# Optimization experiments

Measured on AMD Instinct MI355X. Metric: run time of the kernel, lower is better.

The kernel has to match this reference:

```python
import math
import jax, jax.numpy as jnp
import numpy as np

B = 16; ENC_S = 64; ENC_T = 96
SCALE = 64; POOL = 16; DM = 256; NH = 16
E_LAYERS = 3; D_LAYERS = 2; DFF = 1024
OUT_S = 64; OUT_T = 32
LN_EPS = 1e-5


def _pe(d_model, length):
    pos = np.arange(length, dtype=np.float32)[:, None]
    div = np.exp(np.arange(0, d_model, 2, dtype=np.float32) * (-math.log(10000.0) / d_model))
    pe = np.zeros((length, d_model), np.float32)
    pe[:, 0::2] = np.sin(pos * div)
    pe[:, 1::2] = np.cos(pos * div)
    return jnp.asarray(pe)


def _conv1d_circ(x, w, b):
    # x: (N, C, L), w: (O, C, 3); torch Conv1d(padding=1, padding_mode='circular')
    xp = jnp.pad(x, ((0, 0), (0, 0), (1, 1)), mode='wrap')
    y = jax.lax.conv_general_dilated(xp, w, (1,), 'VALID',
                                     dimension_numbers=('NCH', 'OIH', 'NCH'))
    return y + b[None, :, None]


def _layernorm(x, w, b):
    mu = jnp.mean(x, -1, keepdims=True)
    var = jnp.var(x, -1, keepdims=True)
    return (x - mu) * jax.lax.rsqrt(var + LN_EPS) * w + b


def _data_embedding(x, sproj_w, sproj_b, scproj_w, scproj_b, tok_w, tok_b):
    Bb = x.shape[0]
    h = _conv1d_circ(jnp.swapaxes(x, 1, 2), sproj_w, sproj_b)       # (B, enc_t, enc_t)
    h = _conv1d_circ(h, scproj_w, scproj_b)                          # (B, scale, enc_t)
    h = _conv1d_circ(jnp.swapaxes(h, 1, 2), scproj_w, scproj_b)     # (B, scale, scale)
    h = h.reshape(Bb * SCALE, 1, SCALE)
    tok = jnp.swapaxes(_conv1d_circ(h, tok_w, tok_b), 1, 2)          # (B*scale, scale, dm)
    emb = tok + _pe(DM, SCALE)[None]
    return emb.reshape(Bb, SCALE, SCALE, DM)


def _lin_attn(q, k, v, causal):
    # q,k,v: (Bp, L, H, E); k/v adaptively avg-pooled over L to POOL (L % POOL == 0)
    Bp, L, H, E = q.shape
    win = L // POOL
    kp = k.reshape(Bp, POOL, win, H, E).mean(axis=2)
    vp = v.reshape(Bp, POOL, win, H, E).mean(axis=2)
    scores = jnp.einsum('blhe,bshe->bhls', q, kp)      # (Bp, H, L, POOL)
    if causal:
        m = jnp.arange(POOL)[None, :] > jnp.arange(L)[:, None]
        scores = jnp.where(m[None, None], -jnp.inf, scores)
    A = jax.nn.softmax(scores / math.sqrt(E), axis=-1)
    return jnp.einsum('bhls,bshd->blhd', A, vp)


def _st_attn(x, kv, Wq, bq, Wo, bo, causal):
    Bb, T, S, dm = x.shape
    H = NH // 2
    proj = lambda z: z @ Wq.T + bq
    # faithful to source: query_projection used for q, k AND v; views are flat reshapes
    qt = proj(x.reshape(Bb * S, T, dm)).reshape(Bb * S, T, H, -1)
    qs = proj(x.reshape(Bb * T, S, dm)).reshape(Bb * T, S, H, -1)
    kt = proj(kv.reshape(Bb * S, T, dm)).reshape(Bb * S, T, H, -1)
    ks = proj(kv.reshape(Bb * T, S, dm)).reshape(Bb * T, S, H, -1)
    out_t = _lin_attn(qt, kt, kt, causal).reshape(Bb, S, T, -1)
    out_s = _lin_attn(qs, ks, ks, causal).reshape(Bb, S, T, -1)
    out = jnp.concatenate([out_t, out_s], axis=-1).reshape(Bb, S * T, 2 * dm)
    out = out @ Wo.T + bo
    return out.reshape(Bb, T, S, dm)


def _ffn(x, c1w, c1b, c2w, c2b):
    # conv1d kernel_size=1 over the T axis of (B*S, T, dm) == pointwise GEMM
    Bb, T, S, dm = x.shape
    y = x.reshape(Bb * S, T, dm)
    y = jax.nn.gelu(jnp.einsum('ntd,fd->ntf', y, c1w) + c1b, approximate=False)
    y = jnp.einsum('ntf,df->ntd', y, c2w) + c2b
    return y.reshape(Bb, T, S, dm)


def _forward(x_enc, x_dec,
             enc_sproj_w, enc_sproj_b, enc_scproj_w, enc_scproj_b, enc_tok_w, enc_tok_b,
             dec_sproj_w, dec_sproj_b, dec_scproj_w, dec_scproj_b, dec_tok_w, dec_tok_b,
             e_Wq, e_bq, e_Wo, e_bo, e_c1w, e_c1b, e_c2w, e_c2b,
             e_ln1w, e_ln1b, e_ln2w, e_ln2b, enc_norm_w, enc_norm_b,
             d_sWq, d_sbq, d_sWo, d_sbo, d_cWq, d_cbq, d_cWo, d_cbo,
             d_c1w, d_c1b, d_c2w, d_c2b,
             d_ln1w, d_ln1b, d_ln2w, d_ln2b, d_ln3w, d_ln3b,
             dec_norm_w, dec_norm_b, proj_w, proj_b):
    enc = _data_embedding(x_enc, enc_sproj_w, enc_sproj_b, enc_scproj_w, enc_scproj_b, enc_tok_w, enc_tok_b)
    for i in range(E_LAYERS):
        h = enc + _st_attn(enc, enc, e_Wq[i], e_bq[i], e_Wo[i], e_bo[i], False)
        h = _layernorm(h, e_ln1w[i], e_ln1b[i])
        enc = _layernorm(h + _ffn(h, e_c1w[i], e_c1b[i], e_c2w[i], e_c2b[i]), e_ln2w[i], e_ln2b[i])
    enc = _layernorm(enc, enc_norm_w, enc_norm_b)
    dec = _data_embedding(x_dec, dec_sproj_w, dec_sproj_b, dec_scproj_w, dec_scproj_b, dec_tok_w, dec_tok_b)
    for i in range(D_LAYERS):
        h = dec + _st_attn(dec, dec, d_sWq[i], d_sbq[i], d_sWo[i], d_sbo[i], True)
        h = _layernorm(h, d_ln1w[i], d_ln1b[i])
        h = h + _st_attn(h, enc, d_cWq[i], d_cbq[i], d_cWo[i], d_cbo[i], False)
        h = _layernorm(h, d_ln2w[i], d_ln2b[i])
        dec = _layernorm(h + _ffn(h, d_c1w[i], d_c1b[i], d_c2w[i], d_c2b[i]), d_ln3w[i], d_ln3b[i])
    dec = _layernorm(dec, dec_norm_w, dec_norm_b)
    dec = dec.mean(axis=2)                 # (B, scale, dm)
    out = dec @ proj_w.T + proj_b          # (B, scale, out_s)
    return out[:, -OUT_T:, :]


def setup_inputs() -> dict:
    keys = iter(jax.random.split(jax.random.key(0), 80))
    def nrm(shape, s=0.02):
        return jax.random.normal(next(keys), shape, jnp.float32) * s
    E, D = E_LAYERS, D_LAYERS
    inp = {
        'x_enc': nrm((B, ENC_T, ENC_S), 1.0),
        'x_dec': nrm((B, ENC_T, ENC_S), 1.0),
    }
    for p in ('enc', 'dec'):
        inp[p + '_sproj_w'] = nrm((ENC_T, ENC_S, 3)); inp[p + '_sproj_b'] = nrm((ENC_T,))
        inp[p + '_scproj_w'] = nrm((SCALE, ENC_T, 3)); inp[p + '_scproj_b'] = nrm((SCALE,))
        inp[p + '_tok_w'] = nrm((DM, 1, 3), 0.1); inp[p + '_tok_b'] = nrm((DM,))
    inp.update(
        e_Wq=nrm((E, DM, DM)), e_bq=nrm((E, DM)),
        e_Wo=nrm((E, DM, 2 * DM)), e_bo=nrm((E, DM)),
        e_c1w=nrm((E, DFF, DM)), e_c1b=nrm((E, DFF)),
        e_c2w=nrm((E, DM, DFF)), e_c2b=nrm((E, DM)),
        e_ln1w=jnp.ones((E, DM)), e_ln1b=jnp.zeros((E, DM)),
        e_ln2w=jnp.ones((E, DM)), e_ln2b=jnp.zeros((E, DM)),
        enc_norm_w=jnp.ones((DM,)), enc_norm_b=jnp.zeros((DM,)),
        d_sWq=nrm((D, DM, DM)), d_sbq=nrm((D, DM)),
        d_sWo=nrm((D, DM, 2 * DM)), d_sbo=nrm((D, DM)),
        d_cWq=nrm((D, DM, DM)), d_cbq=nrm((D, DM)),
        d_cWo=nrm((D, DM, 2 * DM)), d_cbo=nrm((D, DM)),
        d_c1w=nrm((D, DFF, DM)), d_c1b=nrm((D, DFF)),
        d_c2w=nrm((D, DM, DFF)), d_c2b=nrm((D, DM)),
        d_ln1w=jnp.ones((D, DM)), d_ln1b=jnp.zeros((D, DM)),
        d_ln2w=jnp.ones((D, DM)), d_ln2b=jnp.zeros((D, DM)),
        d_ln3w=jnp.ones((D, DM)), d_ln3b=jnp.zeros((D, DM)),
        dec_norm_w=jnp.ones((DM,)), dec_norm_b=jnp.zeros((DM,)),
        proj_w=nrm((OUT_S, DM)), proj_b=nrm((OUT_S,)),
    )
    return inp


def reference(x_enc, x_dec,
              enc_sproj_w, enc_sproj_b, enc_scproj_w, enc_scproj_b, enc_tok_w, enc_tok_b,
              dec_sproj_w, dec_sproj_b, dec_scproj_w, dec_scproj_b, dec_tok_w, dec_tok_b,
              e_Wq, e_bq, e_Wo, e_bo, e_c1w, e_c1b, e_c2w, e_c2b,
              e_ln1w, e_ln1b, e_ln2w, e_ln2b, enc_norm_w, enc_norm_b,
              d_sWq, d_sbq, d_sWo, d_sbo, d_cWq, d_cbq, d_cWo, d_cbo,
              d_c1w, d_c1b, d_c2w, d_c2b,
              d_ln1w, d_ln1b, d_ln2w, d_ln2b, d_ln3w, d_ln3b,
              dec_norm_w, dec_norm_b, proj_w, proj_b):
    return _forward(x_enc, x_dec,
                    enc_sproj_w, enc_sproj_b, enc_scproj_w, enc_scproj_b, enc_tok_w, enc_tok_b,
                    dec_sproj_w, dec_sproj_b, dec_scproj_w, dec_scproj_b, dec_tok_w, dec_tok_b,
                    e_Wq, e_bq, e_Wo, e_bo, e_c1w, e_c1b, e_c2w, e_c2b,
                    e_ln1w, e_ln1b, e_ln2w, e_ln2b, enc_norm_w, enc_norm_b,
                    d_sWq, d_sbq, d_sWo, d_sbo, d_cWq, d_cbq, d_cWo, d_cbo,
                    d_c1w, d_c1b, d_c2w, d_c2b,
                    d_ln1w, d_ln1b, d_ln2w, d_ln2b, d_ln3w, d_ln3b,
                    dec_norm_w, dec_norm_b, proj_w, proj_b)
```

## Files before the change

kernel.cpp:

```cpp
#include <hip/hip_runtime.h>


typedef unsigned short u16;
typedef short s16;
typedef __attribute__((ext_vector_type(8))) s16 bfrag;
typedef __attribute__((ext_vector_type(4))) float f32x4;

__device__ __forceinline__ float b2f(u16 u) {
  union { float f; unsigned int i; } v; v.i = ((unsigned int)u) << 16; return v.f;
}
__device__ __forceinline__ u16 f2b(float f) {
  union { float f; unsigned int i; } v; v.f = f;
  unsigned int x = v.i;
  return (u16)((x + 0x7FFFu + ((x >> 16) & 1u)) >> 16);
}
__device__ __forceinline__ float gelu_f(float v) {
  float u = 0.7978845608f * v * (1.0f + 0.044715f * v * v);
  float e = __expf(2.0f * u);
  return v * (1.0f - 1.0f / (e + 1.0f));
}

__device__ __forceinline__ void gload16(const void* g, void* l) {
  __builtin_amdgcn_global_load_lds(
      (const __attribute__((address_space(1))) unsigned int*)g,
      (__attribute__((address_space(3))) unsigned int*)l, 16, 0, 0);
}

__global__ void ws_signal(float* out, float v) { out[0] = v; }

__global__ void cvt_bf(const float* __restrict__ src, u16* __restrict__ dst, int n) {
  int i = blockIdx.x * 256 + threadIdx.x;
  if (i < n) dst[i] = f2b(src[i]);
}
__global__ void weff_bf(const float* __restrict__ Wo, u16* __restrict__ W) {
  int n = blockIdx.x, k = threadIdx.x;
  W[n * 256 + k] = f2b(Wo[n * 512 + k] + Wo[n * 512 + 256 + k]);
}

__global__ void pe_kernel(float* __restrict__ pe) {
  int l = blockIdx.x, d = threadIdx.x;
  int i = d >> 1;
  float div = expf((float)(2 * i) * (-9.210340371976184f / 256.0f));
  float ang = (float)l * div;
  pe[l * 256 + d] = (d & 1) ? cosf(ang) : sinf(ang);
}

__global__ void conv_sproj(const float* __restrict__ x, const float* __restrict__ w,
                           const float* __restrict__ bias, float* __restrict__ h1) {
  int o = blockIdx.x, b = blockIdx.y, l = threadIdx.x;
  const float* wo = w + o * 192;
  const float* xb = x + (size_t)b * 96 * 64;
  float acc = bias[o];
#pragma unroll
  for (int k = 0; k < 3; ++k) {
    int lp = l + k - 1; if (lp < 0) lp += 96; if (lp >= 96) lp -= 96;
    const float* xr = xb + lp * 64;
    for (int c = 0; c < 64; ++c) acc = fmaf(xr[c], wo[c * 3 + k], acc);
  }
  h1[((size_t)b * 96 + o) * 96 + l] = acc;
}

__global__ void conv_scproj_t(const float* __restrict__ h1, const float* __restrict__ w,
                              const float* __restrict__ bias, float* __restrict__ h2) {
  int o = blockIdx.x, b = blockIdx.y, l = threadIdx.x;
  const float* wo = w + o * 288;
  const float* hb = h1 + (size_t)b * 96 * 96;
  float acc = bias[o];
#pragma unroll
  for (int k = 0; k < 3; ++k) {
    int lp = l + k - 1; if (lp < 0) lp += 96; if (lp >= 96) lp -= 96;
    for (int c = 0; c < 96; ++c) acc = fmaf(hb[c * 96 + lp], wo[c * 3 + k], acc);
  }
  h2[((size_t)b * 64 + o) * 96 + l] = acc;
}

__global__ void conv_scproj_s(const float* __restrict__ h2, const float* __restrict__ w,
                              const float* __restrict__ bias, float* __restrict__ h3) {
  int o = blockIdx.x, b = blockIdx.y, l = threadIdx.x;
  const float* wo = w + o * 288;
  const float* hb = h2 + (size_t)b * 64 * 96;
  float acc = bias[o];
#pragma unroll
  for (int k = 0; k < 3; ++k) {
    int lp = l + k - 1; if (lp < 0) lp += 64; if (lp >= 64) lp -= 64;
    for (int c = 0; c < 96; ++c) acc = fmaf(hb[lp * 96 + c], wo[c * 3 + k], acc);
  }
  h3[((size_t)b * 64 + o) * 64 + l] = acc;
}

__global__ void tok_embed(const float* __restrict__ h3, const float* __restrict__ w,
                          const float* __restrict__ bias, const float* __restrict__ pe,
                          u16* __restrict__ E) {
  int g = blockIdx.x, d = threadIdx.x;
  __shared__ float row[64];
  if (d < 64) row[d] = h3[(size_t)g * 64 + d];
  __syncthreads();
  float w0 = w[d * 3], w1 = w[d * 3 + 1], w2 = w[d * 3 + 2], bd = bias[d];
  for (int j = 0; j < 64; ++j) {
    int jm = (j + 63) & 63, jp = (j + 1) & 63;
    float v = bd + row[jm] * w0 + row[j] * w1 + row[jp] * w2 + pe[j * 256 + d];
    E[((size_t)g * 64 + j) * 256 + d] = f2b(v);
  }
}

template <int ACT, int NBX>
__global__ __launch_bounds__(256) void mfma_gemm(const u16* __restrict__ A,
                                                 const u16* __restrict__ W,
                                                 const float* __restrict__ bias,
                                                 u16* __restrict__ C, int N, int K,
                                                 int nby) {
  __shared__ s16 smem[16384];
  s16* Asb[2] = {smem, smem + 4096};
  s16* Bsb[2] = {smem + 8192, smem + 12288};
  constexpr int LB = (NBX == 8) ? 3 : 1;
  int f = blockIdx.x;
  int q = (NBX * nby) >> 3;
  int w = (f & 7) * q + (f >> 3);
  int bx = w & (NBX - 1), by = w >> LB;
  int t = threadIdx.x;
  int wave = t >> 6, lane = t & 63;
  int wr = wave >> 1, wc = wave & 1;
  int row0 = by * 128, col0 = bx * 128;
  int kc = (lane >> 4) & 3, rr = lane & 15;
  const u16* Ap0 = A + (size_t)(row0 + wave * 16 + rr) * K + kc * 8;
  const u16* Ap1 = A + (size_t)(row0 + (wave + 4) * 16 + rr) * K + kc * 8;
  const u16* Bp0 = W + (size_t)(col0 + wave * 16 + rr) * K + kc * 8;
  const u16* Bp1 = W + (size_t)(col0 + (wave + 4) * 16 + rr) * K + kc * 8;
  f32x4 acc[4][4];
#pragma unroll
  for (int m = 0; m < 4; ++m)
#pragma unroll
    for (int n = 0; n < 4; ++n) acc[m][n] = (f32x4){0.f, 0.f, 0.f, 0.f};

  auto STAGE = [&](s16* a, s16* b, int kidx) {
    int k0 = kidx * 32;
    gload16(Ap0 + k0, a + wave * 512);
    gload16(Ap1 + k0, a + (wave + 4) * 512);
    gload16(Bp0 + k0, b + wave * 512);
    gload16(Bp1 + k0, b + (wave + 4) * 512);
  };
  auto COMPUTE = [&](const s16* a, const s16* b) {
    bfrag af[4], bf[4];
#pragma unroll
    for (int m = 0; m < 4; ++m) af[m] = *(const bfrag*)(a + ((wr * 4 + m) * 64 + lane) * 8);
#pragma unroll
    for (int n = 0; n < 4; ++n) bf[n] = *(const bfrag*)(b + ((wc * 4 + n) * 64 + lane) * 8);
#pragma unroll
    for (int m = 0; m < 4; ++m)
#pragma unroll
      for (int n = 0; n < 4; ++n)
        acc[m][n] = __builtin_amdgcn_mfma_f32_16x16x32_bf16(af[m], bf[n], acc[m][n], 0, 0, 0);
  };

  int nk = K >> 5;
  STAGE(Asb[0], Bsb[0], 0);
  __syncthreads();
  for (int ks = 0; ks < nk; ks += 2) {
    if (ks + 1 < nk) STAGE(Asb[1], Bsb[1], ks + 1);
    COMPUTE(Asb[0], Bsb[0]);
    __syncthreads();
    if (ks + 1 < nk) {
      if (ks + 2 < nk) STAGE(Asb[0], Bsb[0], ks + 2);
      COMPUTE(Asb[1], Bsb[1]);
      __syncthreads();
    }
  }
  s16* Cs = smem;
  int g4 = (lane >> 4) << 2;
  int cl = lane & 15;
  float bc[4];
#pragma unroll
  for (int n = 0; n < 4; ++n) bc[n] = bias[col0 + wc * 64 + n * 16 + cl];
#pragma unroll
  for (int P = 0; P < 4; ++P) {
    __syncthreads();
    if (wr == (P >> 1)) {
#pragma unroll
      for (int mm = 0; mm < 2; ++mm) {
        int m = (P & 1) * 2 + mm;
#pragma unroll
        for (int n = 0; n < 4; ++n) {
#pragma unroll
          for (int r = 0; r < 4; ++r) {
            float v = acc[m][n][r] + bc[n];
            if (ACT == 1) v = gelu_f(v);
            Cs[(mm * 16 + g4 + r) * 136 + wc * 64 + n * 16 + cl] = (s16)f2b(v);
          }
        }
      }
    }
    __syncthreads();
#pragma unroll
    for (int it = 0; it < 2; ++it) {
      int idx = it * 256 + t;
      int lr = idx >> 4, slot = idx & 15;
      *(uint4*)(C + (size_t)(row0 + P * 32 + lr) * N + col0 + slot * 8) =
          *(const uint4*)(Cs + lr * 136 + slot * 8);
    }
  }
}

__global__ __launch_bounds__(512) void mfma_gemm_resln(const u16* __restrict__ X,
                                                       const u16* __restrict__ W,
                                                       const float* __restrict__ bias,
                                                       u16* __restrict__ R,
                                                       const float* __restrict__ lnw,
                                                       const float* __restrict__ lnb,
                                                       int K) {
  __shared__ s16 smem[24576];
  __shared__ float pls[32][4][2];
  s16* Asb[2] = {smem, smem + 4096};
  s16* Bsb[2] = {smem + 8192, smem + 16384};
  int t = threadIdx.x;
  int wave = t >> 6, lane = t & 63;
  int wr = wave >> 2, wc = wave & 3;
  int row0 = blockIdx.x * 128;
  int kc = (lane >> 4) & 3, rr = lane & 15;
  const u16* Xp = X + (size_t)(row0 + wave * 16 + rr) * K + kc * 8;
  const u16* Wp0 = W + (size_t)(wave * 16 + rr) * K + kc * 8;
  const u16* Wp1 = W + (size_t)((wave + 8) * 16 + rr) * K + kc * 8;
  f32x4 acc[4][4];
#pragma unroll
  for (int m = 0; m < 4; ++m)
#pragma unroll
    for (int n = 0; n < 4; ++n) acc[m][n] = (f32x4){0.f, 0.f, 0.f, 0.f};

  auto STAGE = [&](s16* a, s16* b, int kidx) {
    int k0 = kidx * 32;
    gload16(Xp + k0, a + wave * 512);
    gload16(Wp0 + k0, b + wave * 512);
    gload16(Wp1 + k0, b + (wave + 8) * 512);
  };
  auto COMPUTE = [&](const s16* a, const s16* b) {
    bfrag af[4], bf[4];
#pragma unroll
    for (int m = 0; m < 4; ++m) af[m] = *(const bfrag*)(a + ((wr * 4 + m) * 64 + lane) * 8);
#pragma unroll
    for (int n = 0; n < 4; ++n) bf[n] = *(const bfrag*)(b + ((wc * 4 + n) * 64 + lane) * 8);
#pragma unroll
    for (int m = 0; m < 4; ++m)
#pragma unroll
      for (int n = 0; n < 4; ++n)
        acc[m][n] = __builtin_amdgcn_mfma_f32_16x16x32_bf16(af[m], bf[n], acc[m][n], 0, 0, 0);
  };

  int nk = K >> 5;
  STAGE(Asb[0], Bsb[0], 0);
  __syncthreads();
  for (int ks = 0; ks < nk; ks += 2) {
    if (ks + 1 < nk) STAGE(Asb[1], Bsb[1], ks + 1);
    COMPUTE(Asb[0], Bsb[0]);
    __syncthreads();
    if (ks + 1 < nk) {
      if (ks + 2 < nk) STAGE(Asb[0], Bsb[0], ks + 2);
      COMPUTE(Asb[1], Bsb[1]);
      __syncthreads();
    }
  }
  s16* Rs = smem;
  int g4 = (lane >> 4) << 2;
  int cl = lane & 15;
  float lw[4], lb[4], bc[4];
#pragma unroll
  for (int n = 0; n < 4; ++n) {
    int col = wc * 64 + n * 16 + cl;
    bc[n] = bias[col]; lw[n] = lnw[col]; lb[n] = lnb[col];
  }
#pragma unroll
  for (int P = 0; P < 4; ++P) {
    bool own = (wr == (P >> 1));
    __syncthreads();
#pragma unroll
    for (int it = 0; it < 2; ++it) {
      int idx = it * 512 + t;
      int lr = idx >> 5, slot = idx & 31;
      *(uint4*)(Rs + lr * 264 + slot * 8) =
          *(const uint4*)(R + (size_t)(row0 + P * 32 + lr) * 256 + slot * 8);
    }
    __syncthreads();
    if (own) {
#pragma unroll
      for (int mm = 0; mm < 2; ++mm) {
        int m = (P & 1) * 2 + mm;
#pragma unroll
        for (int r = 0; r < 4; ++r) {
          int lr = mm * 16 + g4 + r;
          float s = 0.f, s2 = 0.f;
#pragma unroll
          for (int n = 0; n < 4; ++n) {
            float v = acc[m][n][r] + bc[n] +
                      b2f((u16)Rs[lr * 264 + wc * 64 + n * 16 + cl]);
            acc[m][n][r] = v;
            s += v; s2 = fmaf(v, v, s2);
          }
#pragma unroll
          for (int o = 1; o < 16; o <<= 1) { s += __shfl_xor(s, o); s2 += __shfl_xor(s2, o); }
          if (cl == 0) { pls[lr][wc][0] = s; pls[lr][wc][1] = s2; }
        }
      }
    }
    __syncthreads();
    if (own) {
#pragma unroll
      for (int mm = 0; mm < 2; ++mm) {
        int m = (P & 1) * 2 + mm;
#pragma unroll
        for (int r = 0; r < 4; ++r) {
          int lr = mm * 16 + g4 + r;
          float s = pls[lr][0][0] + pls[lr][1][0] + pls[lr][2][0] + pls[lr][3][0];
          float s2 = pls[lr][0][1] + pls[lr][1][1] + pls[lr][2][1] + pls[lr][3][1];
          float mu = s * (1.0f / 256.0f);
          float var = fmaxf(s2 * (1.0f / 256.0f) - mu * mu, 0.0f);
          float rs = rsqrtf(var + 1e-5f);
#pragma unroll
          for (int n = 0; n < 4; ++n) {
            Rs[lr * 264 + wc * 64 + n * 16 + cl] =
                (s16)f2b((acc[m][n][r] - mu) * rs * lw[n] + lb[n]);
          }
        }
      }
    }
    __syncthreads();
#pragma unroll
    for (int it = 0; it < 2; ++it) {
      int idx = it * 512 + t;
      int lr = idx >> 5, slot = idx & 31;
      *(uint4*)(R + (size_t)(row0 + P * 32 + lr) * 256 + slot * 8) =
          *(const uint4*)(Rs + lr * 264 + slot * 8);
    }
  }
}

template <int CROSS, int CAUSAL>
__global__ __launch_bounds__(512) void lin_attn(u16* __restrict__ Q,
                                                const u16* __restrict__ KP) {
  __shared__ u16 qs[64 * 264];
  __shared__ float kpool[16][260];
  int p = blockIdx.x, t = threadIdx.x;
  u16* Qg = Q + (size_t)p * 16384;
#pragma unroll
  for (int i = 0; i < 4; ++i) {
    int idx = i * 512 + t;
    int row = idx >> 5, slot = idx & 31;
    *(uint4*)(qs + row * 264 + slot * 8) = *(const uint4*)(Qg + row * 256 + slot * 8);
  }
  __syncthreads();
  if (CROSS) {
    for (int idx = t; idx < 4096; idx += 512) {
      int s = idx >> 8, d = idx & 255;
      kpool[s][d] = b2f(KP[((size_t)p * 16 + s) * 256 + d]);
    }
  } else {
    for (int idx = t; idx < 4096; idx += 512) {
      int s = idx >> 8, d = idx & 255;
      const u16* b0 = qs + (4 * s) * 264 + d;
      kpool[s][d] = 0.25f * (b2f(b0[0]) + b2f(b0[264]) + b2f(b0[528]) + b2f(b0[792]));
    }
  }
  __syncthreads();
  int h = t >> 6, l = t & 63;
  u16* q = qs + l * 264 + h * 32;
  float qr[32];
#pragma unroll
  for (int e = 0; e < 32; e += 4) {
    ushort4 v = *(const ushort4*)&q[e];
    qr[e] = b2f(v.x); qr[e + 1] = b2f(v.y); qr[e + 2] = b2f(v.z); qr[e + 3] = b2f(v.w);
  }
  float sc[16], mx = -INFINITY;
#pragma unroll
  for (int s = 0; s < 16; ++s) {
    const float* kp = &kpool[s][h * 32];
    float d = 0.f;
#pragma unroll
    for (int e = 0; e < 32; ++e) d = fmaf(qr[e], kp[e], d);
    d *= 0.17677669529663687f;
    if (CAUSAL && s > l) d = -INFINITY;
    sc[s] = d; mx = fmaxf(mx, d);
  }
  float sum = 0.f;
#pragma unroll
  for (int s = 0; s < 16; ++s) { sc[s] = expf(sc[s] - mx); sum += sc[s]; }
  float inv = 1.0f / sum;
  float o[32] = {};
#pragma unroll
  for (int s = 0; s < 16; ++s) {
    float a = sc[s] * inv;
    const float* vp = &kpool[s][h * 32];
#pragma unroll
    for (int e = 0; e < 32; ++e) o[e] = fmaf(a, vp[e], o[e]);
  }
#pragma unroll
  for (int e = 0; e < 32; e += 4) {
    ushort4 v;
    v.x = f2b(o[e]); v.y = f2b(o[e + 1]); v.z = f2b(o[e + 2]); v.w = f2b(o[e + 3]);
    *(ushort4*)&q[e] = v;
  }
  __syncthreads();
#pragma unroll
  for (int i = 0; i < 4; ++i) {
    int idx = i * 512 + t;
    int row = idx >> 5, slot = idx & 31;
    *(uint4*)(Qg + row * 256 + slot * 8) = *(const uint4*)(qs + row * 264 + slot * 8);
  }
}

__global__ __launch_bounds__(256) void ln_bf(u16* __restrict__ X,
                                             const float* __restrict__ w,
                                             const float* __restrict__ b) {
  int lane = threadIdx.x & 63, wv = threadIdx.x >> 6;
  size_t row = (size_t)blockIdx.x * 4 + wv;
  size_t off = row * 256 + lane * 4;
  ushort4 xv = *(const ushort4*)(X + off);
  float v0 = b2f(xv.x), v1 = b2f(xv.y), v2 = b2f(xv.z), v3 = b2f(xv.w);
  float s = v0 + v1 + v2 + v3;
  float s2 = v0 * v0 + v1 * v1 + v2 * v2 + v3 * v3;
#pragma unroll
  for (int o = 32; o; o >>= 1) { s += __shfl_xor(s, o); s2 += __shfl_xor(s2, o); }
  float mu = s * (1.0f / 256.0f);
  float var = fmaxf(s2 * (1.0f / 256.0f) - mu * mu, 0.0f);
  float rs = rsqrtf(var + 1e-5f);
  float4 w4 = *(const float4*)(w + lane * 4);
  float4 b4 = *(const float4*)(b + lane * 4);
  ushort4 o4;
  o4.x = f2b((v0 - mu) * rs * w4.x + b4.x);
  o4.y = f2b((v1 - mu) * rs * w4.y + b4.y);
  o4.z = f2b((v2 - mu) * rs * w4.z + b4.z);
  o4.w = f2b((v3 - mu) * rs * w4.w + b4.w);
  *(ushort4*)(X + off) = o4;
}

__global__ void pool_bf(const u16* __restrict__ A, u16* __restrict__ P) {
  int r = blockIdx.x, d = threadIdx.x;
  int g = r >> 4, s = r & 15;
  const u16* src = A + ((size_t)g * 64 + 4 * (size_t)s) * 256 + d;
  float v = 0.25f * (b2f(src[0]) + b2f(src[256]) + b2f(src[512]) + b2f(src[768]));
  P[(size_t)r * 256 + d] = f2b(v);
}

__global__ __launch_bounds__(256) void mean_proj_bf(const u16* __restrict__ X,
                                                    const float* __restrict__ pw,
                                                    const float* __restrict__ pb,
                                                    float* __restrict__ out) {
  int bid = blockIdx.x;
  int b = bid >> 5, ii = bid & 31;
  int i = 32 + ii;
  __shared__ float md[256];
  int d = threadIdx.x;
  const u16* base = X + ((size_t)b * 64 + i) * 64 * 256 + d;
  float s = 0.f;
  for (int j = 0; j < 64; ++j) s += b2f(base[(size_t)j * 256]);
  md[d] = s * (1.0f / 64.0f);
  __syncthreads();
  if (d < 64) {
    float acc = pb[d];
    const float* wr = pw + d * 256;
    for (int k = 0; k < 256; ++k) acc = fmaf(md[k], wr[k], acc);
    out[((size_t)b * 32 + ii) * 64 + d] = acc;
  }
}

extern "C" void kernel_launch(void* const* d_in, const int* in_sizes, int n_in,
                              void* d_out, int out_size, void* d_ws, size_t ws_size,
                              hipStream_t stream) {
  (void)in_sizes; (void)out_size;
  if (n_in < 50) return;

  const float* x_enc = (const float*)d_in[0];
  const float* x_dec = (const float*)d_in[1];
  const float* enc_sproj_w = (const float*)d_in[2];
  const float* enc_sproj_b = (const float*)d_in[3];
  const float* enc_scproj_w = (const float*)d_in[4];
  const float* enc_scproj_b = (const float*)d_in[5];
  const float* enc_tok_w = (const float*)d_in[6];
  const float* enc_tok_b = (const float*)d_in[7];
  const float* dec_sproj_w = (const float*)d_in[8];
  const float* dec_sproj_b = (const float*)d_in[9];
  const float* dec_scproj_w = (const float*)d_in[10];
  const float* dec_scproj_b = (const float*)d_in[11];
  const float* dec_tok_w = (const float*)d_in[12];
  const float* dec_tok_b = (const float*)d_in[13];
  const float* e_Wq = (const float*)d_in[14];
  const float* e_bq = (const float*)d_in[15];
  const float* e_Wo = (const float*)d_in[16];
  const float* e_bo = (const float*)d_in[17];
  const float* e_c1w = (const float*)d_in[18];
  const float* e_c1b = (const float*)d_in[19];
  const float* e_c2w = (const float*)d_in[20];
  const float* e_c2b = (const float*)d_in[21];
  const float* e_ln1w = (const float*)d_in[22];
  const float* e_ln1b = (const float*)d_in[23];
  const float* e_ln2w = (const float*)d_in[24];
  const float* e_ln2b = (const float*)d_in[25];
  const float* enc_norm_w = (const float*)d_in[26];
  const float* enc_norm_b = (const float*)d_in[27];
  const float* d_sWq = (const float*)d_in[28];
  const float* d_sbq = (const float*)d_in[29];
  const float* d_sWo = (const float*)d_in[30];
  const float* d_sbo = (const float*)d_in[31];
  const float* d_cWq = (const float*)d_in[32];
  const float* d_cbq = (const float*)d_in[33];
  const float* d_cWo = (const float*)d_in[34];
  const float* d_cbo = (const float*)d_in[35];
  const float* d_c1w = (const float*)d_in[36];
  const float* d_c1b = (const float*)d_in[37];
  const float* d_c2w = (const float*)d_in[38];
  const float* d_c2b = (const float*)d_in[39];
  const float* d_ln1w = (const float*)d_in[40];
  const float* d_ln1b = (const float*)d_in[41];
  const float* d_ln2w = (const float*)d_in[42];
  const float* d_ln2b = (const float*)d_in[43];
  const float* d_ln3w = (const float*)d_in[44];
  const float* d_ln3b = (const float*)d_in[45];
  const float* dec_norm_w = (const float*)d_in[46];
  const float* dec_norm_b = (const float*)d_in[47];
  const float* proj_w = (const float*)d_in[48];
  const float* proj_b = (const float*)d_in[49];

  const size_t ACT = 16777216;
  const size_t POOLE = 4194304;
  const size_t WBN = 3538944;
  size_t base_need = (3 * ACT + 2 * POOLE + WBN) * 2 +
                     (size_t)(16384 + 147456 + 98304 + 65536) * 4;
  if (ws_size < base_need) {
    ws_signal<<<1, 1, 0, stream>>>((float*)d_out, (float)(ws_size >> 20));
    return;
  }
  char* wsb = (char*)d_ws;
  u16* A_enc = (u16*)wsb;  wsb += ACT * 2;
  u16* A_dec = (u16*)wsb;  wsb += ACT * 2;
  u16* T1 = (u16*)wsb;     wsb += ACT * 2;
  u16* PA = (u16*)wsb;     wsb += POOLE * 2;
  u16* PK = (u16*)wsb;     wsb += POOLE * 2;
  u16* WB = (u16*)wsb;     wsb += WBN * 2;
  float* PE = (float*)wsb;  wsb += 16384 * 4;
  float* EH1 = (float*)wsb; wsb += 147456 * 4;
  float* EH2 = (float*)wsb; wsb += 98304 * 4;
  float* EH3 = (float*)wsb; wsb += 65536 * 4;

  int hf_rows = 16384;
  u16* HF = T1;
  if (ws_size >= base_need + (size_t)65536 * 1024 * 2) {
    hf_rows = 65536; HF = (u16*)wsb;
  } else if (ws_size >= base_need + (size_t)32768 * 1024 * 2) {
    hf_rows = 32768; HF = (u16*)wsb;
  }

  u16* eWq = WB;
  u16* eWeff = WB + 196608;
  u16* eC1 = WB + 393216;
  u16* eC2 = WB + 1179648;
  u16* dB = WB + 1966080;
  u16* dsWq = dB;
  u16* dsWeff = dB + 131072;
  u16* dcWq = dB + 262144;
  u16* dcWeff = dB + 393216;
  u16* dC1 = dB + 524288;
  u16* dC2 = dB + 1048576;

  cvt_bf<<<768, 256, 0, stream>>>(e_Wq, eWq, 196608);
  cvt_bf<<<3072, 256, 0, stream>>>(e_c1w, eC1, 786432);
  cvt_bf<<<3072, 256, 0, stream>>>(e_c2w, eC2, 786432);
  cvt_bf<<<512, 256, 0, stream>>>(d_sWq, dsWq, 131072);
  cvt_bf<<<512, 256, 0, stream>>>(d_cWq, dcWq, 131072);
  cvt_bf<<<2048, 256, 0, stream>>>(d_c1w, dC1, 524288);
  cvt_bf<<<2048, 256, 0, stream>>>(d_c2w, dC2, 524288);
  for (int i = 0; i < 3; ++i)
    weff_bf<<<256, 256, 0, stream>>>(e_Wo + (size_t)i * 131072, eWeff + (size_t)i * 65536);
  for (int i = 0; i < 2; ++i) {
    weff_bf<<<256, 256, 0, stream>>>(d_sWo + (size_t)i * 131072, dsWeff + (size_t)i * 65536);
    weff_bf<<<256, 256, 0, stream>>>(d_cWo + (size_t)i * 131072, dcWeff + (size_t)i * 65536);
  }

  pe_kernel<<<64, 256, 0, stream>>>(PE);

  conv_sproj<<<dim3(96, 16), 96, 0, stream>>>(x_enc, enc_sproj_w, enc_sproj_b, EH1);
  conv_scproj_t<<<dim3(64, 16), 96, 0, stream>>>(EH1, enc_scproj_w, enc_scproj_b, EH2);
  conv_scproj_s<<<dim3(64, 16), 64, 0, stream>>>(EH2, enc_scproj_w, enc_scproj_b, EH3);
  tok_embed<<<1024, 256, 0, stream>>>(EH3, enc_tok_w, enc_tok_b, PE, A_enc);

  for (int i = 0; i < 3; ++i) {
    mfma_gemm<0, 2><<<1024, 256, 0, stream>>>(A_enc, eWq + (size_t)i * 65536,
                                              e_bq + i * 256, T1, 256, 256, 512);
    lin_attn<0, 0><<<1024, 512, 0, stream>>>(T1, nullptr);
    mfma_gemm_resln<<<512, 512, 0, stream>>>(T1, eWeff + (size_t)i * 65536, e_bo + i * 256,
                                             A_enc, e_ln1w + i * 256, e_ln1b + i * 256, 256);
    for (int m0 = 0; m0 < 65536; m0 += hf_rows) {
      u16* Xc = A_enc + (size_t)m0 * 256;
      int nby = hf_rows / 128;
      mfma_gemm<1, 8><<<8 * nby, 256, 0, stream>>>(
          Xc, eC1 + (size_t)i * 262144, e_c1b + i * 1024, HF, 1024, 256, nby);
      mfma_gemm_resln<<<nby, 512, 0, stream>>>(
          HF, eC2 + (size_t)i * 262144, e_c2b + i * 256, Xc,
          e_ln2w + i * 256, e_ln2b + i * 256, 1024);
    }
  }
  ln_bf<<<16384, 256, 0, stream>>>(A_enc, enc_norm_w, enc_norm_b);
  pool_bf<<<16384, 256, 0, stream>>>(A_enc, PA);

  conv_sproj<<<dim3(96, 16), 96, 0, stream>>>(x_dec, dec_sproj_w, dec_sproj_b, EH1);
  conv_scproj_t<<<dim3(64, 16), 96, 0, stream>>>(EH1, dec_scproj_w, dec_scproj_b, EH2);
  conv_scproj_s<<<dim3(64, 16), 64, 0, stream>>>(EH2, dec_scproj_w, dec_scproj_b, EH3);
  tok_embed<<<1024, 256, 0, stream>>>(EH3, dec_tok_w, dec_tok_b, PE, A_dec);

  for (int i = 0; i < 2; ++i) {
    mfma_gemm<0, 2><<<1024, 256, 0, stream>>>(A_dec, dsWq + (size_t)i * 65536,
                                              d_sbq + i * 256, T1, 256, 256, 512);
    lin_attn<0, 1><<<1024, 512, 0, stream>>>(T1, nullptr);
    mfma_gemm_resln<<<512, 512, 0, stream>>>(T1, dsWeff + (size_t)i * 65536, d_sbo + i * 256,
                                             A_dec, d_ln1w + i * 256, d_ln1b + i * 256, 256);
    mfma_gemm<0, 2><<<1024, 256, 0, stream>>>(A_dec, dcWq + (size_t)i * 65536,
                                              d_cbq + i * 256, T1, 256, 256, 512);
    mfma_gemm<0, 2><<<256, 256, 0, stream>>>(PA, dcWq + (size_t)i * 65536,
                                             d_cbq + i * 256, PK, 256, 256, 128);
    lin_attn<1, 0><<<1024, 512, 0, stream>>>(T1, PK);
    mfma_gemm_resln<<<512, 512, 0, stream>>>(T1, dcWeff + (size_t)i * 65536, d_cbo + i * 256,
                                             A_dec, d_ln2w + i * 256, d_ln2b + i * 256, 256);
    for (int m0 = 0; m0 < 65536; m0 += hf_rows) {
      u16* Xc = A_dec + (size_t)m0 * 256;
      int nby = hf_rows / 128;
      mfma_gemm<1, 8><<<8 * nby, 256, 0, stream>>>(
          Xc, dC1 + (size_t)i * 262144, d_c1b + i * 1024, HF, 1024, 256, nby);
      mfma_gemm_resln<<<nby, 512, 0, stream>>>(
          HF, dC2 + (size_t)i * 262144, d_c2b + i * 256, Xc,
          d_ln3w + i * 256, d_ln3b + i * 256, 1024);
    }
  }
  ln_bf<<<16384, 256, 0, stream>>>(A_dec, dec_norm_w, dec_norm_b);

  mean_proj_bf<<<512, 256, 0, stream>>>(A_dec, proj_w, proj_b, (float*)d_out);
}
```

Before: 1.898 ms.

## Restructure GEMM K-loop into two-ahead prefetch with explicit vmcnt waits

Reworks the main loops of both MFMA GEMM kernels so two k-tiles are in flight. Each step waits only on the older tile's loads via a partial vmcnt, then reads fragments into registers. After a barrier it issues the async load two tiles ahead into the buffer just consumed, and the MFMAs overlap that load. This is meant to hide global-to-LDS latency that the old one-ahead scheme with full __syncthreads exposed, at the cost of relying on hand-counted waitcnt values and assuming nk is even.

```diff
diff --git a/kernel.cpp b/kernel.cpp
--- a/kernel.cpp
+++ b/kernel.cpp
@@ -110,8 +110,8 @@
                                                  u16* __restrict__ C, int N, int K,
                                                  int nby) {
   __shared__ s16 smem[16384];
-  s16* Asb[2] = {smem, smem + 4096};
-  s16* Bsb[2] = {smem + 8192, smem + 12288};
+  s16* A0 = smem;        s16* A1 = smem + 4096;
+  s16* B0 = smem + 8192; s16* B1 = smem + 12288;
   constexpr int LB = (NBX == 8) ? 3 : 1;
   int f = blockIdx.x;
   int q = (NBX * nby) >> 3;
@@ -139,12 +139,23 @@
     gload16(Bp0 + k0, b + wave * 512);
     gload16(Bp1 + k0, b + (wave + 4) * 512);
   };
-  auto COMPUTE = [&](const s16* a, const s16* b) {
+  int nk = K >> 5;
+  auto STEP = [&](const s16* a, const s16* b, s16* sa, s16* sb, int ks) {
+    if (ks + 1 < nk) asm volatile("s_waitcnt vmcnt(4)" ::: "memory");
+    else             asm volatile("s_waitcnt vmcnt(0)" ::: "memory");
+    __builtin_amdgcn_sched_barrier(0);
+    __builtin_amdgcn_s_barrier();
+    __builtin_amdgcn_sched_barrier(0);
     bfrag af[4], bf[4];
 #pragma unroll
     for (int m = 0; m < 4; ++m) af[m] = *(const bfrag*)(a + ((wr * 4 + m) * 64 + lane) * 8);
 #pragma unroll
     for (int n = 0; n < 4; ++n) bf[n] = *(const bfrag*)(b + ((wc * 4 + n) * 64 + lane) * 8);
+    asm volatile("s_waitcnt lgkmcnt(0)" ::: "memory");
+    __builtin_amdgcn_sched_barrier(0);
+    __builtin_amdgcn_s_barrier();
+    __builtin_amdgcn_sched_barrier(0);
+    if (ks + 2 < nk) STAGE(sa, sb, ks + 2);
 #pragma unroll
     for (int m = 0; m < 4; ++m)
 #pragma unroll
@@ -152,18 +163,11 @@
         acc[m][n] = __builtin_amdgcn_mfma_f32_16x16x32_bf16(af[m], bf[n], acc[m][n], 0, 0, 0);
   };
 
-  int nk = K >> 5;
-  STAGE(Asb[0], Bsb[0], 0);
-  __syncthreads();
+  STAGE(A0, B0, 0);
+  STAGE(A1, B1, 1);
   for (int ks = 0; ks < nk; ks += 2) {
-    if (ks + 1 < nk) STAGE(Asb[1], Bsb[1], ks + 1);
-    COMPUTE(Asb[0], Bsb[0]);
-    __syncthreads();
-    if (ks + 1 < nk) {
-      if (ks + 2 < nk) STAGE(Asb[0], Bsb[0], ks + 2);
-      COMPUTE(Asb[1], Bsb[1]);
-      __syncthreads();
-    }
+    STEP(A0, B0, A0, B0, ks);
+    STEP(A1, B1, A1, B1, ks + 1);
   }
   s16* Cs = smem;
   int g4 = (lane >> 4) << 2;
@@ -209,8 +213,8 @@
                                                        int K) {
   __shared__ s16 smem[24576];
   __shared__ float pls[32][4][2];
-  s16* Asb[2] = {smem, smem + 4096};
-  s16* Bsb[2] = {smem + 8192, smem + 16384};
+  s16* A0 = smem;        s16* A1 = smem + 4096;
+  s16* B0 = smem + 8192; s16* B1 = smem + 16384;
   int t = threadIdx.x;
   int wave = t >> 6, lane = t & 63;
   int wr = wave >> 2, wc = wave & 3;
@@ -231,12 +235,23 @@
     gload16(Wp0 + k0, b + wave * 512);
     gload16(Wp1 + k0, b + (wave + 8) * 512);
   };
-  auto COMPUTE = [&](const s16* a, const s16* b) {
+  int nk = K >> 5;
+  auto STEP = [&](const s16* a, const s16* b, s16* sa, s16* sb, int ks) {
+    if (ks + 1 < nk) asm volatile("s_waitcnt vmcnt(3)" ::: "memory");
+    else             asm volatile("s_waitcnt vmcnt(0)" ::: "memory");
+    __builtin_amdgcn_sched_barrier(0);
+    __builtin_amdgcn_s_barrier();
+    __builtin_amdgcn_sched_barrier(0);
     bfrag af[4], bf[4];
 #pragma unroll
     for (int m = 0; m < 4; ++m) af[m] = *(const bfrag*)(a + ((wr * 4 + m) * 64 + lane) * 8);
 #pragma unroll
     for (int n = 0; n < 4; ++n) bf[n] = *(const bfrag*)(b + ((wc * 4 + n) * 64 + lane) * 8);
+    asm volatile("s_waitcnt lgkmcnt(0)" ::: "memory");
+    __builtin_amdgcn_sched_barrier(0);
+    __builtin_amdgcn_s_barrier();
+    __builtin_amdgcn_sched_barrier(0);
+    if (ks + 2 < nk) STAGE(sa, sb, ks + 2);
 #pragma unroll
     for (int m = 0; m < 4; ++m)
 #pragma unroll
@@ -244,18 +259,11 @@
         acc[m][n] = __builtin_amdgcn_mfma_f32_16x16x32_bf16(af[m], bf[n], acc[m][n], 0, 0, 0);
   };
 
-  int nk = K >> 5;
-  STAGE(Asb[0], Bsb[0], 0);
-  __syncthreads();
+  STAGE(A0, B0, 0);
+  STAGE(A1, B1, 1);
   for (int ks = 0; ks < nk; ks += 2) {
-    if (ks + 1 < nk) STAGE(Asb[1], Bsb[1], ks + 1);
-    COMPUTE(Asb[0], Bsb[0]);
-    __syncthreads();
-    if (ks + 1 < nk) {
-      if (ks + 2 < nk) STAGE(Asb[0], Bsb[0], ks + 2);
-      COMPUTE(Asb[1], Bsb[1]);
-      __syncthreads();
-    }
+    STEP(A0, B0, A0, B0, ks);
+    STEP(A1, B1, A1, B1, ks + 1);
   }
   s16* Rs = smem;
   int g4 = (lane >> 4) << 2;
```

Result: faster. 1.792 ms (-5.6%).
